# Kernel tuning notes

Hardware: AMD Instinct MI355X
Metric: run time of the kernel (lower is better)

Reference implementation:

```python
import jax, jax.numpy as jnp
import numpy as np

N, E = 100000, 1000000
HID, EDGE_D, DIST_D, TIME_D, EXTRA = 128, 64, 64, 128, 3
HEADS = 1 + EXTRA
IN_CH = 2 * HID + EDGE_D + DIST_D


def setup_inputs() -> dict:
    key = jax.random.key(0)
    ks = jax.random.split(key, 16)
    inp = {
        "h": jax.random.normal(ks[0], (N, HID), jnp.float32),
        "pos": jax.random.normal(ks[1], (N, 3), jnp.float32),
        "edge_attr": jax.random.normal(ks[2], (E, EDGE_D), jnp.float32),
        "dist": jax.random.normal(ks[3], (E, DIST_D), jnp.float32),
        "time_emb": jax.random.normal(ks[4], (E, TIME_D), jnp.float32),
        "adj_extra": jax.random.uniform(ks[5], (E, EXTRA), jnp.float32),
        # params
        "W_time": jax.random.normal(ks[6], (TIME_D, 2 * HID), jnp.float32) / np.sqrt(TIME_D),
        "b_time": jnp.zeros((2 * HID,), jnp.float32),
        "W_in": jax.random.normal(ks[7], (IN_CH, HID), jnp.float32) / np.sqrt(IN_CH),
        "b_in": jnp.zeros((HID,), jnp.float32),
        "W1": jax.random.normal(ks[8], (HID, HID), jnp.float32) / np.sqrt(HID),
        "b1": jnp.zeros((HID,), jnp.float32),
        "W2": jax.random.normal(ks[9], (HID, HEADS), jnp.float32) / np.sqrt(HID),
        "coors_scale": jnp.full((1,), 0.01, jnp.float32),
        "edge_index": jax.random.randint(ks[10], (2, E), 0, N, jnp.int32),
    }
    return inp


def _layernorm(x, eps=1e-6):
    mu = jnp.mean(x, axis=-1, keepdims=True)
    var = jnp.var(x, axis=-1, keepdims=True)
    return (x - mu) * jax.lax.rsqrt(var + eps)


def reference(h, pos, edge_attr, dist, time_emb, adj_extra,
              W_time, b_time, W_in, b_in, W1, b1, W2, coors_scale,
              edge_index):
    row, col = edge_index[0], edge_index[1]
    # gather node features per edge: [E, 2H+edge+dist]
    h_input = jnp.concatenate([h[row], h[col], edge_attr, dist], axis=1)
    # CoorsNorm(scale_init=0.01)
    coord_diff = pos[row] - pos[col]                       # [E, 3]
    norm = jnp.linalg.norm(coord_diff, axis=-1, keepdims=True)
    coord_diff = coord_diff / jnp.maximum(norm, 1e-8) * coors_scale
    # time conditioning: SiLU -> Linear -> (shift, scale)
    t = jax.nn.silu(time_emb) @ W_time + b_time            # [E, 2H]
    shift, scale = jnp.split(t, 2, axis=1)
    inv = _layernorm(h_input @ W_in + b_in)                # [E, H]
    inv = inv * (1.0 + scale) + shift                      # modulate
    # coord MLP -> per-head scalar, tanh-bounded
    inv = jnp.tanh(jax.nn.silu(inv @ W1 + b1) @ W2)        # [E, heads]
    adjs = jnp.concatenate([jnp.ones((adj_extra.shape[0], 1), inv.dtype), adj_extra], axis=-1)
    inv = jnp.mean(inv * adjs, axis=-1, keepdims=True)     # [E, 1]
    trans = coord_diff * inv                               # [E, 3]
    agg = jax.ops.segment_sum(trans, row, num_segments=pos.shape[0])
    return pos + agg
```

## Files before the change

### kernel.cpp

```cpp
#include <hip/hip_runtime.h>
#include <hip/hip_bf16.h>

#define E_EDGES 1000000
#define N_NODES 100000

typedef __attribute__((ext_vector_type(8))) short bf16x8;
typedef __attribute__((ext_vector_type(4))) float f32x4;

#define WAITV(N) asm volatile("s_waitcnt vmcnt(" #N ")" ::: "memory")
#define WAITL()  asm volatile("s_waitcnt lgkmcnt(0)" ::: "memory")
#define BAR()    __builtin_amdgcn_s_barrier()

__device__ __forceinline__ short f2bf(float f) {
    union { __bf16 b; short s; } u;
    u.b = (__bf16)f;
    return u.s;
}
__device__ __forceinline__ bf16x8 pack8(float4 a, float4 b) {
    bf16x8 r;
    r[0]=f2bf(a.x); r[1]=f2bf(a.y); r[2]=f2bf(a.z); r[3]=f2bf(a.w);
    r[4]=f2bf(b.x); r[5]=f2bf(b.y); r[6]=f2bf(b.z); r[7]=f2bf(b.w);
    return r;
}
__device__ __forceinline__ float4 ld4(const float* p) {
    return *reinterpret_cast<const float4*>(p);
}
__device__ __forceinline__ float silu1(float x) { return x / (1.f + __expf(-x)); }
__device__ __forceinline__ float tanh1(float x) {
    float e = __expf(2.f * x);
    return 1.f - 2.f / (e + 1.f);
}

__global__ void pack_weights_kernel(const float* __restrict__ Wt,
                                    const float* __restrict__ Win,
                                    const float* __restrict__ W1,
                                    const float* __restrict__ W2,
                                    short* __restrict__ ws)
{
    int gid = blockIdx.x * 256 + threadIdx.x;
    if (gid >= 196 * 512) return;
    int frag = gid >> 9, within = gid & 511;
    int l = within >> 3, j = within & 7;
    int lg = l >> 4, ln = l & 15;
    int krow = (lg << 3) + j;
    float v;
    if (frag < 96) {
        int cs = frag >> 3, nt = frag & 7;
        int seg = cs >> 2, ks = cs & 3;
        int base = (seg == 0) ? 256 : (seg == 1) ? 0 : 128;
        int k = base + ks * 32 + krow;
        v = Win[k * 128 + nt * 16 + ln];
    } else if (frag < 160) {
        int t = frag - 96, ch = t >> 3, sub = t & 7;
        int jj = sub >> 2, ks = sub & 3;
        int jcol = (ch < 4) ? (8 + 2 * ch + jj) : (2 * (ch - 4) + jj);
        int k = ks * 32 + krow;
        v = Wt[k * 256 + jcol * 16 + ln];
    } else if (frag < 192) {
        int t = frag - 160, ch = t >> 3, sub = t & 7;
        int nt = 2 * ch + (sub >> 2), ks = sub & 3;
        int k = ks * 32 + krow;
        v = W1[k * 128 + nt * 16 + ln];
    } else {
        int ks = frag - 192;
        int k = ks * 32 + krow;
        v = (ln < 4) ? W2[k * 4 + ln] : 0.0f;
    }
    ws[gid] = f2bf(v);
}

__global__ void h_pack_kernel(const float* __restrict__ h, short* __restrict__ hbf) {
    long i = (long)(blockIdx.x * 256 + threadIdx.x) * 8;
    if (i >= (long)N_NODES * 128) return;
    float4 a = ld4(h + i), b = ld4(h + i + 4);
    *reinterpret_cast<bf16x8*>(hbf + i) = pack8(a, b);
}

__device__ __forceinline__ void stage_frag(const short* gsrc, short* ldst) {
    __builtin_amdgcn_global_load_lds(
        (const __attribute__((address_space(1))) void*)gsrc,
        (__attribute__((address_space(3))) void*)ldst, 16, 0, 0);
}

__device__ __forceinline__ int tswz(int row, int colS) {
    return (row * 64 + colS) ^ ((row & 7) << 3);
}

template<bool HBF>
__global__ __launch_bounds__(256, 3)
void edge_kernel(const float* __restrict__ h,
                 const short* __restrict__ hbf,
                 const float* __restrict__ pos,
                 const float* __restrict__ ea,
                 const float* __restrict__ dst_f,
                 const float* __restrict__ temb,
                 const float* __restrict__ adj,
                 const float* __restrict__ btime,
                 const float* __restrict__ bin,
                 const float* __restrict__ b1,
                 const float* __restrict__ cscale,
                 const int*   __restrict__ ei,
                 const short* __restrict__ ws,
                 float* __restrict__ out)
{
    __shared__ __align__(16) short Wb[3][4096];
    __shared__ float sBias[512];

    const int tid = threadIdx.x;
    const int w   = tid >> 6;
    const int l   = tid & 63;
    const int ln  = l & 15;
    const int lg  = l >> 4;
    const int kb  = lg << 3;
    const int e0w = blockIdx.x * 64 + w * 16;
    const int em  = e0w + ln;

    const int ir = ei[em];
    const int ic = ei[E_EDGES + em];

    #pragma unroll
    for (int i = 0; i < 2; ++i) {
        int idx = tid + i * 256;
        float v = (idx < 128) ? bin[idx] : (idx < 256) ? b1[idx - 128] : btime[idx - 256];
        sBias[idx] = v;
    }
    WAITL();

    #define STAGE8(p) { \
        const short* g_ = ws + (p) * 4096 + (w*2) * 512 + l * 8; \
        short* d_ = &Wb[(p) % 3][(w*2) * 512]; \
        stage_frag(g_, d_); \
        stage_frag(g_ + 512, d_ + 512); }
    #define STAGEW2() { \
        stage_frag(ws + 24 * 4096 + w * 512 + l * 8, &Wb[0][w * 512]); }

    float4 tf[8];
    #pragma unroll
    for (int k2 = 0; k2 < 4; ++k2) {
        const float* q = (k2 < 2) ? (ea    + (long)em*64 + k2*32 + kb)
                                  : (dst_f + (long)em*64 + (k2-2)*32 + kb);
        tf[2*k2]   = ld4(q);
        tf[2*k2+1] = ld4(q + 4);
    }
    bf16x8 af_b[4];
    if (HBF) {
        #pragma unroll
        for (int k2 = 0; k2 < 4; ++k2)
            af_b[k2] = *reinterpret_cast<const bf16x8*>(hbf + (long)ir * 128 + k2*32 + kb);
    } else {
        #pragma unroll
        for (int k2 = 0; k2 < 4; ++k2)
            af_b[k2] = pack8(ld4(h + (long)ir*128 + k2*32 + kb),
                             ld4(h + (long)ir*128 + k2*32 + kb + 4));
    }
    STAGE8(0);
    STAGE8(1);
    if (HBF) { WAITV(8); } else { WAITV(4); }
    bf16x8 af_a[4];
    #pragma unroll
    for (int k2 = 0; k2 < 4; ++k2) af_a[k2] = pack8(tf[2*k2], tf[2*k2+1]);

    f32x4 accX[8];
    #pragma unroll
    for (int i = 0; i < 8; ++i) accX[i] = (f32x4){0.f,0.f,0.f,0.f};
    bf16x8 af_c[4];

    #pragma unroll
    for (int c = 0; c < 12; ++c) {
        if (HBF) {
            if (c == 4 || c == 5) { WAITV(6); } else { WAITV(2); }
        } else {
            if (c == 4 || c == 5) { WAITV(10); } else { WAITV(2); }
        }
        BAR();
        if (c == 11) {
            #pragma unroll
            for (int k2 = 0; k2 < 4; ++k2) {
                tf[2*k2]   = ld4(temb + (long)em * 128 + k2*32 + kb);
                tf[2*k2+1] = ld4(temb + (long)em * 128 + k2*32 + kb + 4);
            }
        }
        STAGE8(c + 2);
        if (c == 3) {
            if (HBF) {
                #pragma unroll
                for (int k2 = 0; k2 < 4; ++k2)
                    af_c[k2] = *reinterpret_cast<const bf16x8*>(hbf + (long)ic * 128 + k2*32 + kb);
            } else {
                #pragma unroll
                for (int k2 = 0; k2 < 4; ++k2)
                    af_c[k2] = pack8(ld4(h + (long)ic*128 + k2*32 + kb),
                                     ld4(h + (long)ic*128 + k2*32 + kb + 4));
            }
        }
        {
            const int ks = c & 3;
            const bf16x8 a_use = (c < 4) ? af_a[ks] : (c < 8) ? af_b[ks] : af_c[ks];
            const short* wb = &Wb[c % 3][0];
            #pragma unroll
            for (int nt = 0; nt < 8; ++nt) {
                bf16x8 b = *reinterpret_cast<const bf16x8*>(&wb[nt*512 + l*8]);
                accX[nt] = __builtin_amdgcn_mfma_f32_16x16x32_bf16(a_use, b, accX[nt], 0, 0, 0);
            }
        }
    }

    #pragma unroll
    for (int nt = 0; nt < 8; ++nt) {
        float bv = sBias[(nt<<4) + ln];
        #pragma unroll
        for (int r = 0; r < 4; ++r) accX[nt][r] += bv;
    }
    #pragma unroll
    for (int r = 0; r < 4; ++r) {
        float p = 0.f, q = 0.f;
        #pragma unroll
        for (int nt = 0; nt < 8; ++nt) { float x = accX[nt][r]; p += x; q += x*x; }
        #pragma unroll
        for (int d2 = 1; d2 < 16; d2 <<= 1) { p += __shfl_xor(p, d2); q += __shfl_xor(q, d2); }
        float mean = p * 0.0078125f;
        float var  = q * 0.0078125f - mean * mean;
        float rstd = rsqrtf(var + 1e-6f);
        #pragma unroll
        for (int nt = 0; nt < 8; ++nt)
            accX[nt][r] = (accX[nt][r] - mean) * rstd;
    }

    WAITV(2);
    bf16x8 ttf[4];
    #pragma unroll
    for (int k2 = 0; k2 < 4; ++k2) {
        float4 va = tf[2*k2], vb = tf[2*k2+1];
        va.x=silu1(va.x); va.y=silu1(va.y); va.z=silu1(va.z); va.w=silu1(va.w);
        vb.x=silu1(vb.x); vb.y=silu1(vb.y); vb.z=silu1(vb.z); vb.w=silu1(vb.w);
        ttf[k2] = pack8(va, vb);
    }

    #pragma unroll
    for (int t = 0; t < 8; ++t) {
        WAITV(2);
        BAR();
        STAGE8(14 + t);
        {
            const short* wb = &Wb[(12 + t) % 3][0];
            #pragma unroll
            for (int jj = 0; jj < 2; ++jj) {
                f32x4 tt = (f32x4){0.f,0.f,0.f,0.f};
                #pragma unroll
                for (int ks = 0; ks < 4; ++ks) {
                    bf16x8 b = *reinterpret_cast<const bf16x8*>(&wb[(jj*4+ks)*512 + l*8]);
                    tt = __builtin_amdgcn_mfma_f32_16x16x32_bf16(ttf[ks], b, tt, 0, 0, 0);
                }
                if (t < 4) {
                    const int jx = 2*t + jj;
                    float bsc = sBias[384 + (jx<<4) + ln];
                    #pragma unroll
                    for (int r = 0; r < 4; ++r) accX[jx][r] *= (1.f + tt[r] + bsc);
                } else {
                    const int jx = 2*(t-4) + jj;
                    float bsh = sBias[256 + (jx<<4) + ln];
                    #pragma unroll
                    for (int r = 0; r < 4; ++r) accX[jx][r] += tt[r] + bsh;
                }
            }
        }
    }

    short* tbW = &Wb[1][w * 1024];
    bf16x8 iaf[4];
    WAITL();
    BAR();
    #pragma unroll
    for (int hp = 0; hp < 2; ++hp) {
        #pragma unroll
        for (int nt4 = 0; nt4 < 4; ++nt4) {
            const int nt = hp*4 + nt4;
            #pragma unroll
            for (int r = 0; r < 4; ++r)
                tbW[tswz((lg<<2) + r, (nt4<<4) + ln)] = f2bf(accX[nt][r]);
        }
        #pragma unroll
        for (int k2 = 0; k2 < 2; ++k2)
            iaf[hp*2 + k2] = *reinterpret_cast<const bf16x8*>(&tbW[tswz(ln, (k2<<5) + kb)]);
    }
    WAITL();

    f32x4 accY[8];
    #pragma unroll
    for (int i = 0; i < 8; ++i) accY[i] = (f32x4){0.f,0.f,0.f,0.f};
    #pragma unroll
    for (int u = 0; u < 4; ++u) {
        if (u < 3) { WAITV(2); } else { WAITV(1); }
        BAR();
        if (u < 2)       { STAGE8(22 + u); }
        else if (u == 2) { STAGEW2(); }
        {
            const short* wb = &Wb[(20 + u) % 3][0];
            #pragma unroll
            for (int s = 0; s < 2; ++s) {
                const int nt = 2*u + s;
                #pragma unroll
                for (int ks = 0; ks < 4; ++ks) {
                    bf16x8 b = *reinterpret_cast<const bf16x8*>(&wb[(s*4+ks)*512 + l*8]);
                    accY[nt] = __builtin_amdgcn_mfma_f32_16x16x32_bf16(iaf[ks], b, accY[nt], 0, 0, 0);
                }
            }
        }
    }

    bf16x8 yaf[4];
    WAITL();
    BAR();
    #pragma unroll
    for (int hp = 0; hp < 2; ++hp) {
        #pragma unroll
        for (int nt4 = 0; nt4 < 4; ++nt4) {
            const int nt = hp*4 + nt4;
            float bv = sBias[128 + (nt<<4) + ln];
            #pragma unroll
            for (int r = 0; r < 4; ++r)
                tbW[tswz((lg<<2) + r, (nt4<<4) + ln)] = f2bf(silu1(accY[nt][r] + bv));
        }
        #pragma unroll
        for (int k2 = 0; k2 < 2; ++k2)
            yaf[hp*2 + k2] = *reinterpret_cast<const bf16x8*>(&tbW[tswz(ln, (k2<<5) + kb)]);
    }

    WAITV(0);
    BAR();
    f32x4 accZ = (f32x4){0.f,0.f,0.f,0.f};
    {
        const short* wb = &Wb[0][0];
        #pragma unroll
        for (int ks = 0; ks < 4; ++ks) {
            bf16x8 b = *reinterpret_cast<const bf16x8*>(&wb[ks*512 + l*8]);
            accZ = __builtin_amdgcn_mfma_f32_16x16x32_bf16(yaf[ks], b, accZ, 0, 0, 0);
        }
    }

    {
        float dx = pos[ir*3+0] - pos[ic*3+0];
        float dy = pos[ir*3+1] - pos[ic*3+1];
        float dz = pos[ir*3+2] - pos[ic*3+2];
        float a0 = adj[em*3+0], a1 = adj[em*3+1], a2 = adj[em*3+2];
        float nrm = sqrtf(dx*dx + dy*dy + dz*dz);
        float sc  = cscale[0] / fmaxf(nrm, 1e-8f);
        float cdx = dx * sc, cdy = dy * sc, cdz = dz * sc;
        #pragma unroll
        for (int r = 0; r < 4; ++r) {
            const int m = (lg<<2) + r;
            float z  = tanh1(accZ[r]);
            float w0 = __shfl(a0, m), w1 = __shfl(a1, m), w2 = __shfl(a2, m);
            int   irm  = __shfl(ir, m);
            float cdxm = __shfl(cdx, m), cdym = __shfl(cdy, m), cdzm = __shfl(cdz, m);
            float wt = (ln == 0) ? 1.0f : (ln == 1 ? w0 : (ln == 2 ? w1 : (ln == 3 ? w2 : 0.0f)));
            float v = z * wt;
            v += __shfl_xor(v, 1);
            v += __shfl_xor(v, 2);
            float s = v * 0.25f;
            if (ln < 3) {
                float cdc = (ln == 0) ? cdxm : (ln == 1 ? cdym : cdzm);
                atomicAdd(&out[(long)irm*3 + ln], cdc * s);
            }
        }
    }
    #undef STAGE8
    #undef STAGEW2
}

extern "C" void kernel_launch(void* const* d_in, const int* in_sizes, int n_in,
                              void* d_out, int out_size, void* d_ws, size_t ws_size,
                              hipStream_t stream) {
    const float* h     = (const float*)d_in[0];
    const float* pos   = (const float*)d_in[1];
    const float* ea    = (const float*)d_in[2];
    const float* dist  = (const float*)d_in[3];
    const float* temb  = (const float*)d_in[4];
    const float* adj   = (const float*)d_in[5];
    const float* Wt    = (const float*)d_in[6];
    const float* bt    = (const float*)d_in[7];
    const float* Win   = (const float*)d_in[8];
    const float* bin   = (const float*)d_in[9];
    const float* W1    = (const float*)d_in[10];
    const float* b1    = (const float*)d_in[11];
    const float* W2    = (const float*)d_in[12];
    const float* cs    = (const float*)d_in[13];
    const int*   ei    = (const int*)d_in[14];
    float*       out   = (float*)d_out;
    short*       ws    = (short*)d_ws;

    const size_t W_SHORTS = 25 * 4096;
    const size_t H_SHORTS = (size_t)N_NODES * 128;
    const bool   use_hbf  = ws_size >= (W_SHORTS + H_SHORTS) * sizeof(short);
    short*       hbf      = ws + W_SHORTS;

    pack_weights_kernel<<<(196*512 + 255) / 256, 256, 0, stream>>>(Wt, Win, W1, W2, ws);
    if (use_hbf)
        h_pack_kernel<<<(int)(H_SHORTS / 8 / 256), 256, 0, stream>>>(h, hbf);
    hipMemcpyAsync(out, pos, (size_t)out_size * sizeof(float),
                   hipMemcpyDeviceToDevice, stream);
    if (use_hbf)
        edge_kernel<true><<<E_EDGES / 64, 256, 0, stream>>>(h, hbf, pos, ea, dist, temb, adj,
                                                            bt, bin, b1, cs, ei, ws, out);
    else
        edge_kernel<false><<<E_EDGES / 64, 256, 0, stream>>>(h, hbf, pos, ea, dist, temb, adj,
                                                             bt, bin, b1, cs, ei, ws, out);
}
```

Measured before the change: 552.8 us.

## Precompute per-node h@W_in projections and gather them per edge

Factors the h[row] and h[col] parts of the input linear layer into a per-node precompute kernel (N×256 bf16 projections via MFMA), so the edge kernel gathers precomputed 128-wide partial sums instead of running those 256 K-rows of matmul per edge. This removes about half the edge-level W_in MFMA work and the raw h gathers, at the cost of an extra node kernel and larger gathered rows (scalar 2-byte loads per lane). It also adds a second rounding of the partial sums to bf16. A fallback path is kept when workspace is too small.

```diff
diff --git a/kernel.cpp b/kernel.cpp
--- a/kernel.cpp
+++ b/kernel.cpp
@@ -30,12 +30,367 @@
     float e = __expf(2.f * x);
     return 1.f - 2.f / (e + 1.f);
 }
-
-__global__ void pack_weights_kernel(const float* __restrict__ Wt,
-                                    const float* __restrict__ Win,
-                                    const float* __restrict__ W1,
-                                    const float* __restrict__ W2,
-                                    short* __restrict__ ws)
+__device__ __forceinline__ float bf2f(unsigned short u) {
+    return __uint_as_float(((unsigned)u) << 16);
+}
+
+__device__ __forceinline__ void stage_frag(const short* gsrc, short* ldst) {
+    __builtin_amdgcn_global_load_lds(
+        (const __attribute__((address_space(1))) void*)gsrc,
+        (__attribute__((address_space(3))) void*)ldst, 16, 0, 0);
+}
+
+__device__ __forceinline__ int tswz(int row, int colS) {
+    return (row * 64 + colS) ^ ((row & 7) << 3);
+}
+
+__global__ void pack_weights_f(const float* __restrict__ Wt,
+                               const float* __restrict__ Win,
+                               const float* __restrict__ W1,
+                               const float* __restrict__ W2,
+                               short* __restrict__ ws)
+{
+    int gid = blockIdx.x * 256 + threadIdx.x;
+    if (gid >= 196 * 512) return;
+    int frag = gid >> 9, within = gid & 511;
+    int l = within >> 3, j = within & 7;
+    int lg = l >> 4, ln = l & 15;
+    int krow = (lg << 3) + j;
+    float v;
+    if (frag < 32) {
+        int ks = frag >> 3, nt = frag & 7;
+        v = Win[(256 + ks * 32 + krow) * 128 + nt * 16 + ln];
+    } else if (frag < 96) {
+        int t = frag - 32, ch = t >> 3, sub = t & 7;
+        int jj = sub >> 2, ks = sub & 3;
+        int jcol = (ch < 4) ? (8 + 2 * ch + jj) : (2 * (ch - 4) + jj);
+        v = Wt[(ks * 32 + krow) * 256 + jcol * 16 + ln];
+    } else if (frag < 128) {
+        int t = frag - 96, ch = t >> 3, sub = t & 7;
+        int nt = 2 * ch + (sub >> 2), ks = sub & 3;
+        v = W1[(ks * 32 + krow) * 128 + nt * 16 + ln];
+    } else if (frag < 132) {
+        int ks = frag - 128;
+        v = (ln < 4) ? W2[(ks * 32 + krow) * 4 + ln] : 0.0f;
+    } else {
+        int q = frag - 132;
+        int ntc = q >> 2, ks = q & 3;
+        int base = (ntc < 8) ? 0 : 128;
+        v = Win[(base + ks * 32 + krow) * 128 + (ntc & 7) * 16 + ln];
+    }
+    ws[gid] = f2bf(v);
+}
+
+__global__ __launch_bounds__(256)
+void hpre_kernel(const float* __restrict__ h, const short* __restrict__ ws,
+                 short* __restrict__ hp)
+{
+    const int tid = threadIdx.x;
+    const int w   = tid >> 6;
+    const int l   = tid & 63;
+    const int ln  = l & 15;
+    const int lg  = l >> 4;
+    const int kb  = lg << 3;
+    const int nb  = blockIdx.x * 64 + w * 16;
+    const int nm  = min(nb + ln, N_NODES - 1);
+
+    bf16x8 af[4];
+    #pragma unroll
+    for (int ks = 0; ks < 4; ++ks)
+        af[ks] = pack8(ld4(h + (long)nm * 128 + ks*32 + kb),
+                       ld4(h + (long)nm * 128 + ks*32 + kb + 4));
+    const short* wsp = ws + 132 * 512;
+    #pragma unroll
+    for (int ntc = 0; ntc < 16; ++ntc) {
+        f32x4 acc = (f32x4){0.f,0.f,0.f,0.f};
+        #pragma unroll
+        for (int ks = 0; ks < 4; ++ks) {
+            bf16x8 b = *reinterpret_cast<const bf16x8*>(&wsp[(ntc*4+ks)*512 + l*8]);
+            acc = __builtin_amdgcn_mfma_f32_16x16x32_bf16(af[ks], b, acc, 0, 0, 0);
+        }
+        #pragma unroll
+        for (int r = 0; r < 4; ++r) {
+            int node = nb + (lg<<2) + r;
+            if (node < N_NODES)
+                hp[(long)node * 256 + ntc*16 + ln] = f2bf(acc[r]);
+        }
+    }
+}
+
+__global__ __launch_bounds__(256, 3)
+void edge_kernel_f(const float* __restrict__ pos,
+                   const float* __restrict__ ea,
+                   const float* __restrict__ dst_f,
+                   const float* __restrict__ temb,
+                   const float* __restrict__ adj,
+                   const float* __restrict__ btime,
+                   const float* __restrict__ bin,
+                   const float* __restrict__ b1,
+                   const float* __restrict__ cscale,
+                   const int*   __restrict__ ei,
+                   const short* __restrict__ ws,
+                   const unsigned short* __restrict__ hp,
+                   float* __restrict__ out)
+{
+    __shared__ __align__(16) short Wb[3][4096];
+    __shared__ float sBias[512];
+
+    const int tid = threadIdx.x;
+    const int w   = tid >> 6;
+    const int l   = tid & 63;
+    const int ln  = l & 15;
+    const int lg  = l >> 4;
+    const int kb  = lg << 3;
+    const int e0w = blockIdx.x * 64 + w * 16;
+    const int em  = e0w + ln;
+
+    const int ir = ei[em];
+    const int ic = ei[E_EDGES + em];
+
+    #pragma unroll
+    for (int i = 0; i < 2; ++i) {
+        int idx = tid + i * 256;
+        float v = (idx < 128) ? bin[idx] : (idx < 256) ? b1[idx - 128] : btime[idx - 256];
+        sBias[idx] = v;
+    }
+    WAITL();
+
+    #define STAGE8(p) { \
+        const short* g_ = ws + (p) * 4096 + (w*2) * 512 + l * 8; \
+        short* d_ = &Wb[(p) % 3][(w*2) * 512]; \
+        stage_frag(g_, d_); \
+        stage_frag(g_ + 512, d_ + 512); }
+    #define STAGEW2() { \
+        stage_frag(ws + 16 * 4096 + w * 512 + l * 8, &Wb[1][w * 512]); }
+
+    int irg[4], icg[4];
+    #pragma unroll
+    for (int r = 0; r < 4; ++r) {
+        irg[r] = __shfl(ir, (lg<<2) + r);
+        icg[r] = __shfl(ic, (lg<<2) + r);
+    }
+
+    unsigned short ga[32], gb[32];
+    #pragma unroll
+    for (int r = 0; r < 4; ++r)
+        #pragma unroll
+        for (int nt = 0; nt < 8; ++nt) {
+            ga[r*8+nt] = hp[(long)irg[r]*256 + (nt<<4) + ln];
+            gb[r*8+nt] = hp[(long)icg[r]*256 + 128 + (nt<<4) + ln];
+        }
+    float4 tf[8];
+    #pragma unroll
+    for (int k2 = 0; k2 < 4; ++k2) {
+        const float* q = (k2 < 2) ? (ea    + (long)em*64 + k2*32 + kb)
+                                  : (dst_f + (long)em*64 + (k2-2)*32 + kb);
+        tf[2*k2]   = ld4(q);
+        tf[2*k2+1] = ld4(q + 4);
+    }
+    STAGE8(0);
+    STAGE8(1);
+    WAITV(4);
+
+    f32x4 accX[8];
+    #pragma unroll
+    for (int r = 0; r < 4; ++r)
+        #pragma unroll
+        for (int nt = 0; nt < 8; ++nt)
+            accX[nt][r] = bf2f(ga[r*8+nt]) + bf2f(gb[r*8+nt]);
+    bf16x8 af_a[4];
+    #pragma unroll
+    for (int k2 = 0; k2 < 4; ++k2) af_a[k2] = pack8(tf[2*k2], tf[2*k2+1]);
+
+    #pragma unroll
+    for (int c = 0; c < 4; ++c) {
+        if (c == 3) { WAITV(10); } else { WAITV(2); }
+        BAR();
+        STAGE8(c + 2);
+        if (c == 2) {
+            #pragma unroll
+            for (int k2 = 0; k2 < 4; ++k2) {
+                tf[2*k2]   = ld4(temb + (long)em * 128 + k2*32 + kb);
+                tf[2*k2+1] = ld4(temb + (long)em * 128 + k2*32 + kb + 4);
+            }
+        }
+        {
+            const short* wb = &Wb[c % 3][0];
+            #pragma unroll
+            for (int nt = 0; nt < 8; ++nt) {
+                bf16x8 b = *reinterpret_cast<const bf16x8*>(&wb[nt*512 + l*8]);
+                accX[nt] = __builtin_amdgcn_mfma_f32_16x16x32_bf16(af_a[c], b, accX[nt], 0, 0, 0);
+            }
+        }
+    }
+
+    #pragma unroll
+    for (int nt = 0; nt < 8; ++nt) {
+        float bv = sBias[(nt<<4) + ln];
+        #pragma unroll
+        for (int r = 0; r < 4; ++r) accX[nt][r] += bv;
+    }
+    #pragma unroll
+    for (int r = 0; r < 4; ++r) {
+        float p = 0.f, q = 0.f;
+        #pragma unroll
+        for (int nt = 0; nt < 8; ++nt) { float x = accX[nt][r]; p += x; q += x*x; }
+        #pragma unroll
+        for (int d2 = 1; d2 < 16; d2 <<= 1) { p += __shfl_xor(p, d2); q += __shfl_xor(q, d2); }
+        float mean = p * 0.0078125f;
+        float var  = q * 0.0078125f - mean * mean;
+        float rstd = rsqrtf(var + 1e-6f);
+        #pragma unroll
+        for (int nt = 0; nt < 8; ++nt)
+            accX[nt][r] = (accX[nt][r] - mean) * rstd;
+    }
+
+    WAITV(2);
+    bf16x8 ttf[4];
+    #pragma unroll
+    for (int k2 = 0; k2 < 4; ++k2) {
+        float4 va = tf[2*k2], vb = tf[2*k2+1];
+        va.x=silu1(va.x); va.y=silu1(va.y); va.z=silu1(va.z); va.w=silu1(va.w);
+        vb.x=silu1(vb.x); vb.y=silu1(vb.y); vb.z=silu1(vb.z); vb.w=silu1(vb.w);
+        ttf[k2] = pack8(va, vb);
+    }
+
+    #pragma unroll
+    for (int t = 0; t < 8; ++t) {
+        WAITV(2);
+        BAR();
+        STAGE8(6 + t);
+        {
+            const short* wb = &Wb[(4 + t) % 3][0];
+            #pragma unroll
+            for (int jj = 0; jj < 2; ++jj) {
+                f32x4 tt = (f32x4){0.f,0.f,0.f,0.f};
+                #pragma unroll
+                for (int ks = 0; ks < 4; ++ks) {
+                    bf16x8 b = *reinterpret_cast<const bf16x8*>(&wb[(jj*4+ks)*512 + l*8]);
+                    tt = __builtin_amdgcn_mfma_f32_16x16x32_bf16(ttf[ks], b, tt, 0, 0, 0);
+                }
+                if (t < 4) {
+                    const int jx = 2*t + jj;
+                    float bsc = sBias[384 + (jx<<4) + ln];
+                    #pragma unroll
+                    for (int r = 0; r < 4; ++r) accX[jx][r] *= (1.f + tt[r] + bsc);
+                } else {
+                    const int jx = 2*(t-4) + jj;
+                    float bsh = sBias[256 + (jx<<4) + ln];
+                    #pragma unroll
+                    for (int r = 0; r < 4; ++r) accX[jx][r] += tt[r] + bsh;
+                }
+            }
+        }
+    }
+
+    short* tbW = &Wb[2][w * 1024];
+    bf16x8 iaf[4];
+    WAITL();
+    BAR();
+    #pragma unroll
+    for (int hpx = 0; hpx < 2; ++hpx) {
+        #pragma unroll
+        for (int nt4 = 0; nt4 < 4; ++nt4) {
+            const int nt = hpx*4 + nt4;
+            #pragma unroll
+            for (int r = 0; r < 4; ++r)
+                tbW[tswz((lg<<2) + r, (nt4<<4) + ln)] = f2bf(accX[nt][r]);
+        }
+        #pragma unroll
+        for (int k2 = 0; k2 < 2; ++k2)
+            iaf[hpx*2 + k2] = *reinterpret_cast<const bf16x8*>(&tbW[tswz(ln, (k2<<5) + kb)]);
+    }
+    WAITL();
+
+    f32x4 accY[8];
+    #pragma unroll
+    for (int i = 0; i < 8; ++i) accY[i] = (f32x4){0.f,0.f,0.f,0.f};
+    #pragma unroll
+    for (int u = 0; u < 4; ++u) {
+        if (u < 3) { WAITV(2); } else { WAITV(1); }
+        BAR();
+        if (u == 0)      { STAGE8(14); }
+        else if (u == 1) { STAGE8(15); }
+        else if (u == 2) { STAGEW2(); }
+        {
+            const short* wb = &Wb[(12 + u) % 3][0];
+            #pragma unroll
+            for (int s = 0; s < 2; ++s) {
+                const int nt = 2*u + s;
+                #pragma unroll
+                for (int ks = 0; ks < 4; ++ks) {
+                    bf16x8 b = *reinterpret_cast<const bf16x8*>(&wb[(s*4+ks)*512 + l*8]);
+                    accY[nt] = __builtin_amdgcn_mfma_f32_16x16x32_bf16(iaf[ks], b, accY[nt], 0, 0, 0);
+                }
+            }
+        }
+    }
+
+    bf16x8 yaf[4];
+    WAITL();
+    BAR();
+    #pragma unroll
+    for (int hpx = 0; hpx < 2; ++hpx) {
+        #pragma unroll
+        for (int nt4 = 0; nt4 < 4; ++nt4) {
+            const int nt = hpx*4 + nt4;
+            float bv = sBias[128 + (nt<<4) + ln];
+            #pragma unroll
+            for (int r = 0; r < 4; ++r)
+                tbW[tswz((lg<<2) + r, (nt4<<4) + ln)] = f2bf(silu1(accY[nt][r] + bv));
+        }
+        #pragma unroll
+        for (int k2 = 0; k2 < 2; ++k2)
+            yaf[hpx*2 + k2] = *reinterpret_cast<const bf16x8*>(&tbW[tswz(ln, (k2<<5) + kb)]);
+    }
+
+    WAITV(0);
+    BAR();
+    f32x4 accZ = (f32x4){0.f,0.f,0.f,0.f};
+    {
+        const short* wb = &Wb[1][0];
+        #pragma unroll
+        for (int ks = 0; ks < 4; ++ks) {
+            bf16x8 b = *reinterpret_cast<const bf16x8*>(&wb[ks*512 + l*8]);
+            accZ = __builtin_amdgcn_mfma_f32_16x16x32_bf16(yaf[ks], b, accZ, 0, 0, 0);
+        }
+    }
+
+    {
+        float dx = pos[ir*3+0] - pos[ic*3+0];
+        float dy = pos[ir*3+1] - pos[ic*3+1];
+        float dz = pos[ir*3+2] - pos[ic*3+2];
+        float a0 = adj[em*3+0], a1 = adj[em*3+1], a2 = adj[em*3+2];
+        float nrm = sqrtf(dx*dx + dy*dy + dz*dz);
+        float sc  = cscale[0] / fmaxf(nrm, 1e-8f);
+        float cdx = dx * sc, cdy = dy * sc, cdz = dz * sc;
+        #pragma unroll
+        for (int r = 0; r < 4; ++r) {
+            const int m = (lg<<2) + r;
+            float z  = tanh1(accZ[r]);
+            float w0 = __shfl(a0, m), w1 = __shfl(a1, m), w2 = __shfl(a2, m);
+            int   irm  = __shfl(ir, m);
+            float cdxm = __shfl(cdx, m), cdym = __shfl(cdy, m), cdzm = __shfl(cdz, m);
+            float wt = (ln == 0) ? 1.0f : (ln == 1 ? w0 : (ln == 2 ? w1 : (ln == 3 ? w2 : 0.0f)));
+            float v = z * wt;
+            v += __shfl_xor(v, 1);
+            v += __shfl_xor(v, 2);
+            float s = v * 0.25f;
+            if (ln < 3) {
+                float cdc = (ln == 0) ? cdxm : (ln == 1 ? cdym : cdzm);
+                atomicAdd(&out[(long)irm*3 + ln], cdc * s);
+            }
+        }
+    }
+    #undef STAGE8
+    #undef STAGEW2
+}
+
+__global__ void pack_weights_fb(const float* __restrict__ Wt,
+                                const float* __restrict__ Win,
+                                const float* __restrict__ W1,
+                                const float* __restrict__ W2,
+                                short* __restrict__ ws)
 {
     int gid = blockIdx.x * 256 + threadIdx.x;
     if (gid >= 196 * 512) return;
@@ -76,32 +431,22 @@
     *reinterpret_cast<bf16x8*>(hbf + i) = pack8(a, b);
 }
 
-__device__ __forceinline__ void stage_frag(const short* gsrc, short* ldst) {
-    __builtin_amdgcn_global_load_lds(
-        (const __attribute__((address_space(1))) void*)gsrc,
-        (__attribute__((address_space(3))) void*)ldst, 16, 0, 0);
-}
-
-__device__ __forceinline__ int tswz(int row, int colS) {
-    return (row * 64 + colS) ^ ((row & 7) << 3);
-}
-
 template<bool HBF>
 __global__ __launch_bounds__(256, 3)
-void edge_kernel(const float* __restrict__ h,
-                 const short* __restrict__ hbf,
-                 const float* __restrict__ pos,
-                 const float* __restrict__ ea,
-                 const float* __restrict__ dst_f,
-                 const float* __restrict__ temb,
-                 const float* __restrict__ adj,
-                 const float* __restrict__ btime,
-                 const float* __restrict__ bin,
-                 const float* __restrict__ b1,
-                 const float* __restrict__ cscale,
-                 const int*   __restrict__ ei,
-                 const short* __restrict__ ws,
-                 float* __restrict__ out)
+void edge_kernel_fb(const float* __restrict__ h,
+                    const short* __restrict__ hbf,
+                    const float* __restrict__ pos,
+                    const float* __restrict__ ea,
+                    const float* __restrict__ dst_f,
+                    const float* __restrict__ temb,
+                    const float* __restrict__ adj,
+                    const float* __restrict__ btime,
+                    const float* __restrict__ bin,
+                    const float* __restrict__ b1,
+                    const float* __restrict__ cscale,
+                    const int*   __restrict__ ei,
+                    const short* __restrict__ ws,
+                    float* __restrict__ out)
 {
     __shared__ __align__(16) short Wb[3][4096];
     __shared__ float sBias[512];
@@ -271,17 +616,17 @@
     WAITL();
     BAR();
     #pragma unroll
-    for (int hp = 0; hp < 2; ++hp) {
+    for (int hpx = 0; hpx < 2; ++hpx) {
         #pragma unroll
         for (int nt4 = 0; nt4 < 4; ++nt4) {
-            const int nt = hp*4 + nt4;
+            const int nt = hpx*4 + nt4;
             #pragma unroll
             for (int r = 0; r < 4; ++r)
                 tbW[tswz((lg<<2) + r, (nt4<<4) + ln)] = f2bf(accX[nt][r]);
         }
         #pragma unroll
         for (int k2 = 0; k2 < 2; ++k2)
-            iaf[hp*2 + k2] = *reinterpret_cast<const bf16x8*>(&tbW[tswz(ln, (k2<<5) + kb)]);
+            iaf[hpx*2 + k2] = *reinterpret_cast<const bf16x8*>(&tbW[tswz(ln, (k2<<5) + kb)]);
     }
     WAITL();
 
@@ -312,10 +657,10 @@
     WAITL();
     BAR();
     #pragma unroll
-    for (int hp = 0; hp < 2; ++hp) {
+    for (int hpx = 0; hpx < 2; ++hpx) {
         #pragma unroll
         for (int nt4 = 0; nt4 < 4; ++nt4) {
-            const int nt = hp*4 + nt4;
+            const int nt = hpx*4 + nt4;
             float bv = sBias[128 + (nt<<4) + ln];
             #pragma unroll
             for (int r = 0; r < 4; ++r)
@@ -323,7 +668,7 @@
         }
         #pragma unroll
         for (int k2 = 0; k2 < 2; ++k2)
-            yaf[hp*2 + k2] = *reinterpret_cast<const bf16x8*>(&tbW[tswz(ln, (k2<<5) + kb)]);
+            yaf[hpx*2 + k2] = *reinterpret_cast<const bf16x8*>(&tbW[tswz(ln, (k2<<5) + kb)]);
     }
 
     WAITV(0);
@@ -389,20 +734,32 @@
     float*       out   = (float*)d_out;
     short*       ws    = (short*)d_ws;
 
-    const size_t W_SHORTS = 25 * 4096;
-    const size_t H_SHORTS = (size_t)N_NODES * 128;
-    const bool   use_hbf  = ws_size >= (W_SHORTS + H_SHORTS) * sizeof(short);
-    short*       hbf      = ws + W_SHORTS;
-
-    pack_weights_kernel<<<(196*512 + 255) / 256, 256, 0, stream>>>(Wt, Win, W1, W2, ws);
-    if (use_hbf)
-        h_pack_kernel<<<(int)(H_SHORTS / 8 / 256), 256, 0, stream>>>(h, hbf);
+    const size_t WF_SHORTS = 196 * 512;
+    const size_t HP_SHORTS = (size_t)N_NODES * 256;
+    const size_t HB_SHORTS = (size_t)N_NODES * 128;
+    const bool factored = ws_size >= (WF_SHORTS + HP_SHORTS) * sizeof(short);
+
     hipMemcpyAsync(out, pos, (size_t)out_size * sizeof(float),
                    hipMemcpyDeviceToDevice, stream);
-    if (use_hbf)
-        edge_kernel<true><<<E_EDGES / 64, 256, 0, stream>>>(h, hbf, pos, ea, dist, temb, adj,
-                                                            bt, bin, b1, cs, ei, ws, out);
-    else
-        edge_kernel<false><<<E_EDGES / 64, 256, 0, stream>>>(h, hbf, pos, ea, dist, temb, adj,
-                                                             bt, bin, b1, cs, ei, ws, out);
-}
+
+    if (factored) {
+        short* hp = ws + WF_SHORTS;
+        pack_weights_f<<<(196*512 + 255) / 256, 256, 0, stream>>>(Wt, Win, W1, W2, ws);
+        hpre_kernel<<<(N_NODES + 63) / 64, 256, 0, stream>>>(h, ws, hp);
+        edge_kernel_f<<<E_EDGES / 64, 256, 0, stream>>>(
+            pos, ea, dist, temb, adj, bt, bin, b1, cs, ei, ws,
+            (const unsigned short*)hp, out);
+    } else {
+        const bool use_hbf = ws_size >= (WF_SHORTS + HB_SHORTS) * sizeof(short);
+        short* hbf = ws + WF_SHORTS;
+        pack_weights_fb<<<(196*512 + 255) / 256, 256, 0, stream>>>(Wt, Win, W1, W2, ws);
+        if (use_hbf) {
+            h_pack_kernel<<<(int)(HB_SHORTS / 8 / 256), 256, 0, stream>>>(h, hbf);
+            edge_kernel_fb<true><<<E_EDGES / 64, 256, 0, stream>>>(
+                h, hbf, pos, ea, dist, temb, adj, bt, bin, b1, cs, ei, ws, out);
+        } else {
+            edge_kernel_fb<false><<<E_EDGES / 64, 256, 0, stream>>>(
+                h, hbf, pos, ea, dist, temb, adj, bt, bin, b1, cs, ei, ws, out);
+        }
+    }
+}
```

Result: faster. 525.9 us (-4.9%).
